# Performance work log

Hardware: AMD Instinct MI355X
Metric: run time of the kernel (lower is better)

The kernel has to match this reference:

```python
import jax, jax.numpy as jnp
import numpy as np

B, S, D = 4, 1024, 1280
H, DH = 20, 64          # n_head, d_hidden = embed_dim // n_head
DF = 4 * D              # r_ff = 4


def setup_inputs() -> dict:
    key = jax.random.key(0)
    ks = jax.random.split(key, 8)
    s_qkv = 1.0 / np.sqrt(D)
    inp = {
        "x": jax.random.normal(ks[0], (B, S, D), dtype=jnp.float32),
        # projection weights stored [in, out] so y = x @ W
        "Wq": jax.random.normal(ks[1], (D, H * DH), dtype=jnp.float32) * s_qkv,
        "Wk": jax.random.normal(ks[2], (D, H * DH), dtype=jnp.float32) * s_qkv,
        "Wv": jax.random.normal(ks[3], (D, H * DH), dtype=jnp.float32) * s_qkv,
        "ln_g": jnp.ones((D,), dtype=jnp.float32),
        "ln_b": jnp.zeros((D,), dtype=jnp.float32),
        "W1": jax.random.normal(ks[4], (D, DF), dtype=jnp.float32) * np.sqrt(2.0 / D),
        "b1": jnp.zeros((DF,), dtype=jnp.float32),
        "W2": jax.random.normal(ks[5], (DF, D), dtype=jnp.float32) * (1.0 / np.sqrt(DF)),
        "b2": jnp.zeros((D,), dtype=jnp.float32),
    }
    return inp


def reference(x, Wq, Wk, Wv, ln_g, ln_b, W1, b1, W2, b2):
    scaling = 1.0 / np.sqrt(DH)
    # --- Attention (note: original forward never applies to_out) ---
    q = (x @ Wq).reshape(B, S, H, DH) * scaling
    k = (x @ Wk).reshape(B, S, H, DH)
    v = (x @ Wv).reshape(B, S, H, DH)
    attn = jnp.einsum('bqhd,bkhd->bhqk', q, k)
    attn = jax.nn.softmax(attn, axis=-1)
    out = jnp.einsum('bhqk,bkhd->bqhd', attn, v).reshape(B, S, H * DH)
    x = out + x  # residual
    # --- FeedForward: LayerNorm -> linear1 -> relu -> linear2, residual ---
    mu = jnp.mean(x, axis=-1, keepdims=True)
    var = jnp.mean(jnp.square(x - mu), axis=-1, keepdims=True)
    h = (x - mu) * jax.lax.rsqrt(var + 1e-5) * ln_g + ln_b
    h = jax.nn.relu(h @ W1 + b1)
    h = h @ W2 + b2
    return x + h
```

## Files before the change

### kernel.cpp

```cpp
#include <hip/hip_runtime.h>
#include <hip/hip_bf16.h>

typedef short bf16x8 __attribute__((ext_vector_type(8)));
typedef float f32x4 __attribute__((ext_vector_type(4)));

typedef unsigned int u32_as1 __attribute__((address_space(1)));
typedef unsigned int u32_as3 __attribute__((address_space(3)));

#define B_ 4
#define S_ 1024
#define D_ 1280
#define H_ 20
#define DH_ 64
#define DF_ 5120
#define BS_ (B_*S_)
#define NQKV 3840

__device__ __forceinline__ void gld_lds16(const __hip_bfloat16* g, __hip_bfloat16* l) {
  __builtin_amdgcn_global_load_lds((const u32_as1*)g, (u32_as3*)l, 16, 0, 0);
}

__global__ __launch_bounds__(256) void cvt_f2b(
    const float* __restrict__ in, __hip_bfloat16* __restrict__ out, int n4)
{
  int i = blockIdx.x * 256 + threadIdx.x;
  if (i >= n4) return;
  const float4 v = ((const float4*)in)[i];
  __hip_bfloat16 o[4] = {__float2bfloat16(v.x), __float2bfloat16(v.y),
                         __float2bfloat16(v.z), __float2bfloat16(v.w)};
  *(short4*)(out + (size_t)i * 4) = *(short4*)o;
}

__global__ __launch_bounds__(256) void transpose_f2b(
    const float* __restrict__ in, __hip_bfloat16* __restrict__ out,
    int K, int N)
{
  __shared__ float tile[32][33];
  int k0 = blockIdx.x * 32, n0 = blockIdx.y * 32;
  int tx = threadIdx.x & 31, ty = threadIdx.x >> 5;
  #pragma unroll
  for (int i = 0; i < 32; i += 8)
    tile[ty + i][tx] = in[(size_t)(k0 + ty + i) * N + n0 + tx];
  __syncthreads();
  #pragma unroll
  for (int i = 0; i < 32; i += 8)
    out[(size_t)(n0 + ty + i) * K + k0 + tx] = __float2bfloat16(tile[tx][ty + i]);
}

__global__ __launch_bounds__(256) void transpose_qkv3(
    const float* __restrict__ Wq, const float* __restrict__ Wk,
    const float* __restrict__ Wv, __hip_bfloat16* __restrict__ out)
{
  __shared__ float tile[32][33];
  const int z = blockIdx.z;
  const float* in = (z == 0) ? Wq : ((z == 1) ? Wk : Wv);
  __hip_bfloat16* o = out + (size_t)z * D_ * D_;
  int k0 = blockIdx.x * 32, n0 = blockIdx.y * 32;
  int tx = threadIdx.x & 31, ty = threadIdx.x >> 5;
  #pragma unroll
  for (int i = 0; i < 32; i += 8)
    tile[ty + i][tx] = in[(size_t)(k0 + ty + i) * D_ + n0 + tx];
  __syncthreads();
  #pragma unroll
  for (int i = 0; i < 32; i += 8)
    o[(size_t)(n0 + ty + i) * D_ + k0 + tx] = __float2bfloat16(tile[tx][ty + i]);
}

__global__ __launch_bounds__(256) void transpose_v(
    const __hip_bfloat16* __restrict__ qkv, __hip_bfloat16* __restrict__ vT)
{
  __shared__ __hip_bfloat16 tile[32][33];
  int s0 = blockIdx.x * 32;
  int d0 = blockIdx.y * 32;
  int bh = blockIdx.z;
  int b = bh / H_, h = bh - b * H_;
  int tx = threadIdx.x & 31, ty = threadIdx.x >> 5;
  const __hip_bfloat16* src = qkv + (size_t)b * S_ * NQKV + 2 * D_ + h * DH_;
  #pragma unroll
  for (int i = 0; i < 32; i += 8)
    tile[ty + i][tx] = src[(size_t)(s0 + ty + i) * NQKV + d0 + tx];
  __syncthreads();
  __hip_bfloat16* dst = vT + (size_t)bh * DH_ * S_;
  #pragma unroll
  for (int i = 0; i < 32; i += 8)
    dst[(size_t)(d0 + ty + i) * S_ + s0 + tx] = tile[tx][ty + i];
}

template<int EPI>
__global__ __launch_bounds__(512, 2) void gemm256(
    const __hip_bfloat16* __restrict__ A,
    const __hip_bfloat16* __restrict__ BT,
    const float* __restrict__ bias,
    __hip_bfloat16* __restrict__ C,
    float* __restrict__ Cf0,
    float* __restrict__ Cf1,
    float* __restrict__ Cf2,
    int M, int N, int K, int KextA, int KextR)
{
  __shared__ __align__(16) __hip_bfloat16 As[2][2][256 * 32];
  __shared__ __align__(16) __hip_bfloat16 Bs[2][2][256 * 32];
  __hip_bfloat16* AsF = &As[0][0][0];
  __hip_bfloat16* BsF = &Bs[0][0][0];

  const int t = threadIdx.x;
  const int lane = t & 63;
  const int wave = t >> 6;
  const int wm = wave >> 2, wn = wave & 3;
  const int quad = lane >> 4, l16 = lane & 15;

  const int gx = gridDim.x;
  const int nwg = gx * gridDim.y;
  int orig = blockIdx.y * gx + blockIdx.x;
  int bx = blockIdx.x, by = blockIdx.y;
  if ((nwg & 7) == 0) {
    const int q = nwg >> 3;
    const int swz = (orig & 7) * q + (orig >> 3);
    bx = swz % gx; by = swz / gx;
  }
  const int bm = bx * 256, bn = by * 256;

  const int z = blockIdx.z;
  const int koff = (z == 0) ? 0 : (KextA + (z - 1) * KextR);
  const int Kc = (z == 0) ? KextA : KextR;
  const int NT = Kc >> 6;

  const int srow = t >> 2;
  const int sc = (t & 3) ^ ((t >> 3) & 3);
  const __hip_bfloat16* Ag = A  + (size_t)(bm + srow) * K + koff + sc * 8;
  const __hip_bfloat16* Bg = BT + (size_t)(bn + srow) * K + koff + sc * 8;
  const size_t rq = (size_t)128 * K;

  const int swzf = quad ^ ((l16 >> 1) & 3);
  const int aob = (wm * 128 + l16) * 32 + swzf * 8;
  const int bob = (wn * 64 + l16) * 32 + swzf * 8;

  f32x4 acc[8][4];
  #pragma unroll
  for (int i = 0; i < 8; i++)
    #pragma unroll
    for (int j = 0; j < 4; j++)
      acc[i][j] = (f32x4){0.f, 0.f, 0.f, 0.f};

#define STAGE_A(u_, kk_, b_) do { \
    const __hip_bfloat16* g_ = Ag + (size_t)(u_) * 64 + (kk_) * 32; \
    gld_lds16(g_,      AsF + ((b_) * 2 + (kk_)) * 8192 + t * 8); \
    gld_lds16(g_ + rq, AsF + ((b_) * 2 + (kk_)) * 8192 + 4096 + t * 8); \
  } while (0)
#define STAGE_B(u_, kk_, b_) do { \
    const __hip_bfloat16* g_ = Bg + (size_t)(u_) * 64 + (kk_) * 32; \
    gld_lds16(g_,      BsF + ((b_) * 2 + (kk_)) * 8192 + t * 8); \
    gld_lds16(g_ + rq, BsF + ((b_) * 2 + (kk_)) * 8192 + 4096 + t * 8); \
  } while (0)

  STAGE_A(0, 0, 0); STAGE_B(0, 0, 0); STAGE_A(0, 1, 0); STAGE_B(0, 1, 0);
  STAGE_B(1, 0, 1); STAGE_A(1, 0, 1); STAGE_B(1, 1, 1);
  asm volatile("s_waitcnt vmcnt(6)" ::: "memory");
  __builtin_amdgcn_s_barrier();
  asm volatile("" ::: "memory");

  bf16x8 av[4], bv[4];

#define PHASE_MFMA(ibase_) \
    __builtin_amdgcn_s_barrier(); \
    __builtin_amdgcn_s_setprio(1); \
    _Pragma("unroll") \
    for (int i = 0; i < 4; i++) \
      _Pragma("unroll") \
      for (int j = 0; j < 4; j++) \
        acc[(ibase_) + i][j] = __builtin_amdgcn_mfma_f32_16x16x32_bf16(av[i], bv[j], acc[(ibase_) + i][j], 0, 0, 0); \
    __builtin_amdgcn_s_setprio(0); \
    __builtin_amdgcn_s_barrier(); \
    asm volatile("" ::: "memory");

#define TILE_BODY(u_, B_) do { \
    const int hb0 = (B_) * 2 * 8192, hb1 = ((B_) * 2 + 1) * 8192; \
     \
    _Pragma("unroll") \
    for (int i = 0; i < 4; i++) av[i] = *(const bf16x8*)(AsF + hb0 + aob + i * 512); \
    _Pragma("unroll") \
    for (int j = 0; j < 4; j++) bv[j] = *(const bf16x8*)(BsF + hb0 + bob + j * 512); \
    if ((u_) + 1 < NT) STAGE_A((u_) + 1, 1, (B_) ^ 1); \
    PHASE_MFMA(0) \
     \
    _Pragma("unroll") \
    for (int i = 0; i < 4; i++) av[i] = *(const bf16x8*)(AsF + hb0 + aob + (i + 4) * 512); \
    if ((u_) + 2 < NT) STAGE_B((u_) + 2, 0, (B_)); \
    PHASE_MFMA(4) \
     \
    _Pragma("unroll") \
    for (int i = 0; i < 4; i++) av[i] = *(const bf16x8*)(AsF + hb1 + aob + i * 512); \
    _Pragma("unroll") \
    for (int j = 0; j < 4; j++) bv[j] = *(const bf16x8*)(BsF + hb1 + bob + j * 512); \
    if ((u_) + 2 < NT) STAGE_A((u_) + 2, 0, (B_)); \
    PHASE_MFMA(0) \
     \
    _Pragma("unroll") \
    for (int i = 0; i < 4; i++) av[i] = *(const bf16x8*)(AsF + hb1 + aob + (i + 4) * 512); \
    if ((u_) + 2 < NT) { \
      STAGE_B((u_) + 2, 1, (B_)); \
      asm volatile("s_waitcnt vmcnt(6)" ::: "memory"); \
    } else { \
      asm volatile("s_waitcnt vmcnt(0)" ::: "memory"); \
    } \
    PHASE_MFMA(4) \
  } while (0)

  for (int u = 0; u < NT; u += 2) {
    TILE_BODY(u, 0);
    TILE_BODY(u + 1, 1);
  }

#undef TILE_BODY
#undef PHASE_MFMA
#undef STAGE_A
#undef STAGE_B

  float* Cf = (z == 0) ? Cf0 : ((z == 1) ? Cf1 : Cf2);
  #pragma unroll
  for (int i = 0; i < 8; i++) {
    #pragma unroll
    for (int j = 0; j < 4; j++) {
      int col = bn + wn * 64 + j * 16 + l16;
      #pragma unroll
      for (int r = 0; r < 4; r++) {
        int row = bm + wm * 128 + i * 16 + quad * 4 + r;
        float v = acc[i][j][r];
        if (EPI == 1) { v += bias[col]; v = fmaxf(v, 0.f); }
        if (EPI == 3) {
          Cf[(size_t)row * N + col] = v;
        } else {
          C[(size_t)row * N + col] = __float2bfloat16(v);
        }
      }
    }
  }
}

__global__ __launch_bounds__(256) void ffn2_reduce3(
    const float* __restrict__ P0, const float* __restrict__ P1,
    const float* __restrict__ bias, const float* __restrict__ resid,
    float* __restrict__ out)
{
  int i = blockIdx.x * 256 + threadIdx.x;
  float4 p0 = ((const float4*)P0)[i];
  float4 p1 = ((const float4*)P1)[i];
  float4 p2 = ((const float4*)out)[i];
  float4 r  = ((const float4*)resid)[i];
  float4 b  = ((const float4*)bias)[i % (D_ / 4)];
  float4 o;
  o.x = p0.x + p1.x + p2.x + r.x + b.x;
  o.y = p0.y + p1.y + p2.y + r.y + b.y;
  o.z = p0.z + p1.z + p2.z + r.z + b.z;
  o.w = p0.w + p1.w + p2.w + r.w + b.w;
  ((float4*)out)[i] = o;
}

__global__ __launch_bounds__(256) void attn_mfma(
    const __hip_bfloat16* __restrict__ qkv,
    const __hip_bfloat16* __restrict__ vT,
    const float* __restrict__ x,
    float* __restrict__ x1)
{
  const int qt = blockIdx.x, h = blockIdx.y, b = blockIdx.z;
  const int t = threadIdx.x;
  const int lane = t & 63;
  const int wave = t >> 6;
  const int quad = lane >> 4, l16 = lane & 15;

  __shared__ __hip_bfloat16 Ks[2][64 * 64];
  __shared__ __hip_bfloat16 Vs[2][64 * 64];
  __shared__ short Pl[4][16][72];

  const int qrow0 = qt * 128 + wave * 32;
  const size_t tok0 = (size_t)b * S_;
  const int qcol = h * DH_;
  const int kcol = D_ + h * DH_;
  const size_t vtbase = (size_t)(b * H_ + h) * DH_ * S_;

  const int s1i = t + 256;
  const int r0 = t >> 3,   c0 = (t & 7)   ^ (r0 & 7);
  const int r1 = s1i >> 3, c1 = (s1i & 7) ^ (r1 & 7);
  const __hip_bfloat16* Kg0 = qkv + (tok0 + r0) * NQKV + kcol + c0 * 8;
  const __hip_bfloat16* Kg1 = qkv + (tok0 + r1) * NQKV + kcol + c1 * 8;
  const __hip_bfloat16* Vg0 = vT + vtbase + (size_t)r0 * S_ + c0 * 8;
  const __hip_bfloat16* Vg1 = vT + vtbase + (size_t)r1 * S_ + c1 * 8;
  const size_t kstep = (size_t)64 * NQKV;

  const float qscale = 0.125f * 1.44269504088896340736f;
  bf16x8 aq[2][2];
  #pragma unroll
  for (int m = 0; m < 2; m++)
    #pragma unroll
    for (int kc = 0; kc < 2; kc++) {
      bf16x8 raw = *(const bf16x8*)(qkv + (tok0 + qrow0 + m * 16 + l16) * NQKV
                                        + qcol + kc * 32 + quad * 8);
      bf16x8 scaled;
      #pragma unroll
      for (int j = 0; j < 8; j++) {
        float f = __uint_as_float(((unsigned)(unsigned short)raw[j]) << 16) * qscale;
        __hip_bfloat16 hb = __float2bfloat16(f);
        scaled[j] = *reinterpret_cast<short*>(&hb);
      }
      aq[m][kc] = scaled;
    }

  f32x4 O[2][4];
  float lsum[2][4];
  #pragma unroll
  for (int m = 0; m < 2; m++)
    #pragma unroll
    for (int n = 0; n < 4; n++) O[m][n] = (f32x4){0.f, 0.f, 0.f, 0.f};
  #pragma unroll
  for (int m = 0; m < 2; m++)
    #pragma unroll
    for (int r = 0; r < 4; r++) lsum[m][r] = 0.f;

  gld_lds16(Kg0, &Ks[0][t * 8]);
  gld_lds16(Kg1, &Ks[0][t * 8 + 2048]);
  gld_lds16(Vg0, &Vs[0][t * 8]);
  gld_lds16(Vg1, &Vs[0][t * 8 + 2048]);

  const int fsw = l16 & 7;

  for (int kt = 0; kt < S_ / 64; kt++) {
    const int buf = kt & 1;
    __syncthreads();

    if (kt + 1 < S_ / 64) {
      const int nb = buf ^ 1;
      gld_lds16(Kg0 + (size_t)(kt + 1) * kstep, &Ks[nb][t * 8]);
      gld_lds16(Kg1 + (size_t)(kt + 1) * kstep, &Ks[nb][t * 8 + 2048]);
      gld_lds16(Vg0 + (kt + 1) * 64, &Vs[nb][t * 8]);
      gld_lds16(Vg1 + (kt + 1) * 64, &Vs[nb][t * 8 + 2048]);
    }

    bf16x8 kb[4][2];
    #pragma unroll
    for (int j = 0; j < 4; j++)
      #pragma unroll
      for (int kc = 0; kc < 2; kc++)
        kb[j][kc] = *(const bf16x8*)&Ks[buf][(j * 16 + l16) * 64
                                            + (((kc * 4 + quad) ^ fsw) * 8)];
    f32x4 sc[2][4];
    #pragma unroll
    for (int m = 0; m < 2; m++)
      #pragma unroll
      for (int j = 0; j < 4; j++) {
        sc[m][j] = (f32x4){0.f, 0.f, 0.f, 0.f};
        sc[m][j] = __builtin_amdgcn_mfma_f32_16x16x32_bf16(aq[m][0], kb[j][0], sc[m][j], 0, 0, 0);
        sc[m][j] = __builtin_amdgcn_mfma_f32_16x16x32_bf16(aq[m][1], kb[j][1], sc[m][j], 0, 0, 0);
      }

    bf16x8 vb[4][2];
    #pragma unroll
    for (int n = 0; n < 4; n++)
      #pragma unroll
      for (int kc = 0; kc < 2; kc++)
        vb[n][kc] = *(const bf16x8*)&Vs[buf][(n * 16 + l16) * 64
                                            + (((kc * 4 + quad) ^ fsw) * 8)];

    #pragma unroll
    for (int m = 0; m < 2; m++) {
      #pragma unroll
      for (int j = 0; j < 4; j++)
        #pragma unroll
        for (int r = 0; r < 4; r++) {
          float p = exp2f(sc[m][j][r]);
          lsum[m][r] += p;
          Pl[wave][quad * 4 + r][j * 16 + l16] = (short)(__float_as_uint(p) >> 16);
        }
      bf16x8 pa0 = *(const bf16x8*)&Pl[wave][l16][quad * 8];
      bf16x8 pa1 = *(const bf16x8*)&Pl[wave][l16][32 + quad * 8];
      #pragma unroll
      for (int n = 0; n < 4; n++) {
        O[m][n] = __builtin_amdgcn_mfma_f32_16x16x32_bf16(pa0, vb[n][0], O[m][n], 0, 0, 0);
        O[m][n] = __builtin_amdgcn_mfma_f32_16x16x32_bf16(pa1, vb[n][1], O[m][n], 0, 0, 0);
      }
    }
  }

  #pragma unroll
  for (int m = 0; m < 2; m++)
    #pragma unroll
    for (int r = 0; r < 4; r++) {
      float s = lsum[m][r];
      s += __shfl_xor(s, 1);
      s += __shfl_xor(s, 2);
      s += __shfl_xor(s, 4);
      s += __shfl_xor(s, 8);
      lsum[m][r] = 1.f / s;
    }

  #pragma unroll
  for (int m = 0; m < 2; m++)
    #pragma unroll
    for (int n = 0; n < 4; n++)
      #pragma unroll
      for (int r = 0; r < 4; r++) {
        size_t row = tok0 + qrow0 + m * 16 + quad * 4 + r;
        int col = qcol + n * 16 + l16;
        size_t idx = row * D_ + col;
        x1[idx] = O[m][n][r] * lsum[m][r] + x[idx];
      }
}

__global__ __launch_bounds__(256) void ln_kernel(
    const float* __restrict__ x1, const float* __restrict__ g,
    const float* __restrict__ bta, __hip_bfloat16* __restrict__ h)
{
  int row = blockIdx.x, t = threadIdx.x;
  __shared__ float red[256];
  float v[5];
  size_t base = (size_t)row * D_;
  #pragma unroll
  for (int i = 0; i < 5; i++) v[i] = x1[base + t + 256 * i];
  float s = v[0] + v[1] + v[2] + v[3] + v[4];
  red[t] = s; __syncthreads();
  for (int off = 128; off; off >>= 1) {
    if (t < off) red[t] += red[t + off];
    __syncthreads();
  }
  float mu = red[0] * (1.f / D_);
  __syncthreads();
  float sq = 0.f;
  #pragma unroll
  for (int i = 0; i < 5; i++) { float d = v[i] - mu; sq += d * d; }
  red[t] = sq; __syncthreads();
  for (int off = 128; off; off >>= 1) {
    if (t < off) red[t] += red[t + off];
    __syncthreads();
  }
  float rs = rsqrtf(red[0] * (1.f / D_) + 1e-5f);
  #pragma unroll
  for (int i = 0; i < 5; i++) {
    int c = t + 256 * i;
    float hv = (v[i] - mu) * rs * g[c] + bta[c];
    h[base + c] = __float2bfloat16(hv);
  }
}

extern "C" void kernel_launch(void* const* d_in, const int* in_sizes, int n_in,
                              void* d_out, int out_size, void* d_ws, size_t ws_size,
                              hipStream_t stream) {
  (void)in_sizes; (void)n_in; (void)out_size; (void)ws_size;
  const float* x   = (const float*)d_in[0];
  const float* Wq  = (const float*)d_in[1];
  const float* Wk  = (const float*)d_in[2];
  const float* Wv  = (const float*)d_in[3];
  const float* lng = (const float*)d_in[4];
  const float* lnb = (const float*)d_in[5];
  const float* W1  = (const float*)d_in[6];
  const float* b1  = (const float*)d_in[7];
  const float* W2  = (const float*)d_in[8];
  const float* b2  = (const float*)d_in[9];
  float* out = (float*)d_out;

  char* ws = (char*)d_ws;
  size_t o = 0;
  __hip_bfloat16* W2T = (__hip_bfloat16*)(ws + o); o += (size_t)D_ * DF_ * 2;
  float*          x1  = (float*)(ws + o);          o += (size_t)BS_ * D_ * 4;
  char* regA = ws + o; o += (size_t)DF_ * D_ * 2 + (size_t)BS_ * D_ * 2;
  __hip_bfloat16* W1T  = (__hip_bfloat16*)regA;
  __hip_bfloat16* hbuf = (__hip_bfloat16*)(regA + (size_t)DF_ * D_ * 2);
  float*          P0   = (float*)regA;
  char* regB = ws + o;
  __hip_bfloat16* xb    = (__hip_bfloat16*)regB;
  __hip_bfloat16* BTqkv = (__hip_bfloat16*)(regB + (size_t)BS_ * D_ * 2);
  __hip_bfloat16* qkv   = (__hip_bfloat16*)(regB + (size_t)BS_ * D_ * 2
                                                 + (size_t)NQKV * D_ * 2);
  __hip_bfloat16* vT    = (__hip_bfloat16*)(regB + (size_t)BS_ * D_ * 2
                                                 + (size_t)NQKV * D_ * 2
                                                 + (size_t)BS_ * NQKV * 2);
  float*          P1    = (float*)regB;
  __hip_bfloat16* gbuf  = (__hip_bfloat16*)(regB + (size_t)BS_ * D_ * 4);
  float*          P2    = out;

  transpose_qkv3<<<dim3(D_/32, D_/32, 3), 256, 0, stream>>>(Wq, Wk, Wv, BTqkv);
  transpose_f2b<<<dim3(D_/32, DF_/32), 256, 0, stream>>>(W1, W1T, D_, DF_);
  transpose_f2b<<<dim3(DF_/32, D_/32), 256, 0, stream>>>(W2, W2T, DF_, D_);
  cvt_f2b<<<(BS_*D_/4 + 255)/256, 256, 0, stream>>>(x, xb, BS_*D_/4);

  gemm256<0><<<dim3(BS_/256, NQKV/256), 512, 0, stream>>>(
      xb, BTqkv, nullptr, qkv, nullptr, nullptr, nullptr, BS_, NQKV, D_, D_, D_);
  transpose_v<<<dim3(S_/32, DH_/32, B_*H_), 256, 0, stream>>>(qkv, vT);
  attn_mfma<<<dim3(S_/128, H_, B_), 256, 0, stream>>>(qkv, vT, x, x1);
  ln_kernel<<<BS_, 256, 0, stream>>>(x1, lng, lnb, hbuf);
  gemm256<1><<<dim3(BS_/256, DF_/256), 512, 0, stream>>>(
      hbuf, W1T, b1, gbuf, nullptr, nullptr, nullptr, BS_, DF_, D_, D_, D_);
  gemm256<3><<<dim3(BS_/256, D_/256, 3), 512, 0, stream>>>(
      gbuf, W2T, nullptr, nullptr, P0, P1, P2, BS_, D_, DF_, 1792, 1664);
  ffn2_reduce3<<<BS_*D_/4/256, 256, 0, stream>>>(P0, P1, b2, x1, out);
}
```

Measured before the change: 415.1 us.

## Split FFN1 GEMM tail into split-K small-tile kernel to balance waves

The first FFN GEMM now covers only the first 4096 output columns with the large 256x256 tile kernel. The last 1024 columns are computed by a new 128x128 tile kernel using split-K over two halves, writing fp32 partials into reused buffers. A reduce kernel adds bias, applies ReLU and writes bf16. The intent is to avoid a poorly filled final wave of large tiles, at the cost of an extra launch, extra partial-sum traffic and a less pipelined tile kernel.

```diff
diff --git a/kernel.cpp b/kernel.cpp
--- a/kernel.cpp
+++ b/kernel.cpp
@@ -236,6 +236,105 @@
   }
 }
 
+template<int EPI>
+__global__ __launch_bounds__(256) void gemm_lds(
+    const __hip_bfloat16* __restrict__ A,
+    const __hip_bfloat16* __restrict__ BT,
+    const float* __restrict__ bias,
+    __hip_bfloat16* __restrict__ C,
+    float* __restrict__ Cf0,
+    float* __restrict__ Cf1,
+    int M, int N, int K, int Kext)
+{
+  __shared__ __hip_bfloat16 As[128 * 32];
+  __shared__ __hip_bfloat16 Bs[128 * 32];
+
+  const int t = threadIdx.x;
+  const int lane = t & 63;
+  const int wave = t >> 6;
+  const int wm = wave >> 1, wn = wave & 1;
+  const int bm = blockIdx.x * 128, bn = blockIdx.y * 128;
+  const int quad = lane >> 4, l16 = lane & 15;
+  const int koff = blockIdx.z * Kext;
+
+  const int srow = t >> 2;
+  const int gc = (t & 3) ^ ((srow >> 1) & 3);
+  const __hip_bfloat16* Ag = A  + (size_t)(bm + srow) * K + koff + gc * 8;
+  const __hip_bfloat16* Bg = BT + (size_t)(bn + srow) * K + koff + gc * 8;
+  const size_t rstep = (size_t)64 * K;
+  __hip_bfloat16* Asl = As + t * 8;
+  __hip_bfloat16* Bsl = Bs + t * 8;
+
+  const int rsw = (l16 >> 1) & 3;
+  const int rc = (quad ^ rsw) * 8;
+
+  f32x4 acc[4][4];
+  #pragma unroll
+  for (int i = 0; i < 4; i++)
+    #pragma unroll
+    for (int j = 0; j < 4; j++)
+      acc[i][j] = (f32x4){0.f, 0.f, 0.f, 0.f};
+
+  for (int k0 = 0; k0 < Kext; k0 += 32) {
+    gld_lds16(Ag + k0,         Asl);
+    gld_lds16(Ag + rstep + k0, Asl + 2048);
+    gld_lds16(Bg + k0,         Bsl);
+    gld_lds16(Bg + rstep + k0, Bsl + 2048);
+    __syncthreads();
+
+    bf16x8 a[4], b[4];
+    #pragma unroll
+    for (int i = 0; i < 4; i++)
+      a[i] = *(const bf16x8*)(As + (wm * 64 + i * 16 + l16) * 32 + rc);
+    #pragma unroll
+    for (int j = 0; j < 4; j++)
+      b[j] = *(const bf16x8*)(Bs + (wn * 64 + j * 16 + l16) * 32 + rc);
+    #pragma unroll
+    for (int i = 0; i < 4; i++)
+      #pragma unroll
+      for (int j = 0; j < 4; j++)
+        acc[i][j] = __builtin_amdgcn_mfma_f32_16x16x32_bf16(a[i], b[j], acc[i][j], 0, 0, 0);
+    __syncthreads();
+  }
+
+  float* Cf = (blockIdx.z == 0) ? Cf0 : Cf1;
+  #pragma unroll
+  for (int i = 0; i < 4; i++) {
+    #pragma unroll
+    for (int j = 0; j < 4; j++) {
+      int col = bn + wn * 64 + j * 16 + l16;
+      #pragma unroll
+      for (int r = 0; r < 4; r++) {
+        int row = bm + wm * 64 + i * 16 + quad * 4 + r;
+        float v = acc[i][j][r];
+        if (EPI == 1) { v += bias[col]; v = fmaxf(v, 0.f); }
+        if (EPI == 3) {
+          Cf[(size_t)row * N + col] = v;
+        } else {
+          C[(size_t)row * N + col] = __float2bfloat16(v);
+        }
+      }
+    }
+  }
+}
+
+__global__ __launch_bounds__(256) void ffn1_tail_reduce(
+    const float* __restrict__ P0, const float* __restrict__ P1,
+    const float* __restrict__ bias, __hip_bfloat16* __restrict__ g)
+{
+  int i = blockIdx.x * 256 + threadIdx.x;
+  int row = i >> 8, c4 = i & 255;
+  float4 p0 = ((const float4*)P0)[i];
+  float4 p1 = ((const float4*)P1)[i];
+  float4 b  = ((const float4*)(bias + 4096))[c4];
+  __hip_bfloat16 o[4];
+  o[0] = __float2bfloat16(fmaxf(p0.x + p1.x + b.x, 0.f));
+  o[1] = __float2bfloat16(fmaxf(p0.y + p1.y + b.y, 0.f));
+  o[2] = __float2bfloat16(fmaxf(p0.z + p1.z + b.z, 0.f));
+  o[3] = __float2bfloat16(fmaxf(p0.w + p1.w + b.w, 0.f));
+  *(short4*)(g + (size_t)row * DF_ + 4096 + c4 * 4) = *(short4*)o;
+}
+
 __global__ __launch_bounds__(256) void ffn2_reduce3(
     const float* __restrict__ P0, const float* __restrict__ P1,
     const float* __restrict__ bias, const float* __restrict__ resid,
@@ -472,6 +571,8 @@
                                                  + (size_t)NQKV * D_ * 2
                                                  + (size_t)BS_ * NQKV * 2);
   float*          P1    = (float*)regB;
+  float*          PB0   = (float*)regB;
+  float*          PB1   = out;
   __hip_bfloat16* gbuf  = (__hip_bfloat16*)(regB + (size_t)BS_ * D_ * 4);
   float*          P2    = out;
 
@@ -485,8 +586,14 @@
   transpose_v<<<dim3(S_/32, DH_/32, B_*H_), 256, 0, stream>>>(qkv, vT);
   attn_mfma<<<dim3(S_/128, H_, B_), 256, 0, stream>>>(qkv, vT, x, x1);
   ln_kernel<<<BS_, 256, 0, stream>>>(x1, lng, lnb, hbuf);
-  gemm256<1><<<dim3(BS_/256, DF_/256), 512, 0, stream>>>(
+
+  gemm256<1><<<dim3(BS_/256, 16), 512, 0, stream>>>(
       hbuf, W1T, b1, gbuf, nullptr, nullptr, nullptr, BS_, DF_, D_, D_, D_);
+  gemm_lds<3><<<dim3(BS_/128, 8, 2), 256, 0, stream>>>(
+      hbuf, W1T + (size_t)4096 * D_, nullptr, nullptr, PB0, PB1,
+      BS_, 1024, D_, D_/2);
+  ffn1_tail_reduce<<<BS_*1024/4/256, 256, 0, stream>>>(PB0, PB1, b1, gbuf);
+
   gemm256<3><<<dim3(BS_/256, D_/256, 3), 512, 0, stream>>>(
       gbuf, W2T, nullptr, nullptr, P0, P1, P2, BS_, D_, DF_, 1792, 1664);
   ffn2_reduce3<<<BS_*D_/4/256, 256, 0, stream>>>(P0, P1, b2, x1, out);
```

Result: faster. 404.8 us (-2.5%).
